# Optimization experiments

Measured on AMD Instinct MI355X. Metric: run time of the kernel, lower is better.

## Reference

```python
import jax, jax.numpy as jnp
import numpy as np

EPS = 1e-5
GROUPS = 32

def group_norm(x, w, b):
    B, C, H, W = x.shape
    g = GROUPS
    xr = x.reshape(B, g, C // g, H * W)
    mean = xr.mean(axis=(2, 3), keepdims=True)
    var = xr.var(axis=(2, 3), keepdims=True)
    h = ((xr - mean) / jnp.sqrt(var + EPS)).reshape(B, C, H, W)
    return h * w[None, :, None, None] + b[None, :, None, None]

def setup_inputs() -> dict:
    key = jax.random.key(0)
    ks = jax.random.split(key, 7)
    B, C, H, W = 8, 256, 64, 64
    d = C // 8  # 32
    x = jax.random.normal(ks[0], (B, C, H, W), dtype=jnp.float32)
    norm_w = 1.0 + 0.1 * jax.random.normal(ks[1], (C,), dtype=jnp.float32)
    norm_b = 0.1 * jax.random.normal(ks[2], (C,), dtype=jnp.float32)
    s = 1.0 / np.sqrt(C)
    Wq = jax.random.normal(ks[3], (d, C), dtype=jnp.float32) * s
    Wk = jax.random.normal(ks[4], (d, C), dtype=jnp.float32) * s
    Wv = jax.random.normal(ks[5], (C, C), dtype=jnp.float32) * s
    Wproj = jax.random.normal(ks[6], (C, C), dtype=jnp.float32) * s
    gamma = jnp.full((1,), 0.5, dtype=jnp.float32)  # torch init is 0; nonzero so attention path contributes
    return {"x": x, "norm_w": norm_w, "norm_b": norm_b, "Wq": Wq, "Wk": Wk,
            "Wv": Wv, "Wproj": Wproj, "gamma": gamma}

def reference(x, norm_w, norm_b, Wq, Wk, Wv, Wproj, gamma):
    B, C, H, W = x.shape
    N = H * W
    h = group_norm(x, norm_w, norm_b)           # (B,C,H,W)
    hf = h.reshape(B, C, N)                      # flatten spatial
    d = Wq.shape[0]
    q = jnp.einsum('dc,bcn->bnd', Wq, hf)        # (B,N,d)
    k = jnp.einsum('dc,bcn->bdn', Wk, hf)        # (B,d,N)
    v = jnp.einsum('oc,bcn->bno', Wv, hf)        # (B,N,C)
    scale = d ** (-0.5)
    attn = jax.nn.softmax(jnp.einsum('bnd,bdm->bnm', q, k) * scale, axis=-1)  # (B,N,N)
    out = jnp.einsum('bnm,bmo->bno', attn, v)    # (B,N,C)
    out = out.transpose(0, 2, 1).reshape(B, C, H, W)
    proj = jnp.einsum('oc,bchw->bohw', Wproj, out)
    return x + gamma[0] * proj
```

## Files before the change

kernel.cpp:

```cpp
#include <hip/hip_runtime.h>
#include <cstdint>


typedef __bf16 bf16x8 __attribute__((ext_vector_type(8)));
typedef float f32x4 __attribute__((ext_vector_type(4)));
typedef float f32x16 __attribute__((ext_vector_type(16)));
typedef unsigned int u32x4 __attribute__((ext_vector_type(4)));
typedef unsigned short u16x4 __attribute__((ext_vector_type(4)));
typedef unsigned short u16x8 __attribute__((ext_vector_type(8)));

#define DEVI __device__ __forceinline__

DEVI unsigned short f2bf(float f) {
    __bf16 h = (__bf16)f;
    return __builtin_bit_cast(unsigned short, h);
}
DEVI float bf2f(unsigned short u) {
    unsigned int x = ((unsigned int)u) << 16;
    return __builtin_bit_cast(float, x);
}

DEVI f32x4 mfma16(bf16x8 a, bf16x8 b, f32x4 c) {
    return __builtin_amdgcn_mfma_f32_16x16x32_bf16(a, b, c, 0, 0, 0);
}
DEVI f32x16 mfma32(bf16x8 a, bf16x8 b, f32x16 c) {
    return __builtin_amdgcn_mfma_f32_32x32x16_bf16(a, b, c, 0, 0, 0);
}

DEVI void glds16(const unsigned short* g, unsigned short* l) {
    const __attribute__((address_space(1))) unsigned int* gp =
        reinterpret_cast<const __attribute__((address_space(1))) unsigned int*>(
            reinterpret_cast<uintptr_t>(g));
    __attribute__((address_space(3))) unsigned int* lp =
        reinterpret_cast<__attribute__((address_space(3))) unsigned int*>(
            reinterpret_cast<uintptr_t>(l));
    __builtin_amdgcn_global_load_lds(gp, lp, 16, 0, 0);
}

DEVI void barrier_raw() {
    asm volatile("" ::: "memory");
    __builtin_amdgcn_s_barrier();
    asm volatile("" ::: "memory");
}
DEVI void wait_vm0() {
    __builtin_amdgcn_s_waitcnt(0x3F70);
}

#define QSCALE 0.2550663133f
#define MFIX   12.0f

__global__ __launch_bounds__(1024) void k_gnorm(
        const float* __restrict__ x, const float* __restrict__ gw,
        const float* __restrict__ gb, unsigned short* __restrict__ ht) {
    int bg = blockIdx.x;
    int b = bg >> 5, g = bg & 31;
    const float* xb = x + ((size_t)(b * 256 + g * 8)) * 4096;
    int t = threadIdx.x;
    int n0 = t * 4;
    f32x4 cv[8];
    #pragma unroll
    for (int c = 0; c < 8; c++) cv[c] = *(const f32x4*)(xb + c * 4096 + n0);
    float s1 = 0.f, s2 = 0.f;
    #pragma unroll
    for (int c = 0; c < 8; c++) {
        #pragma unroll
        for (int j = 0; j < 4; j++) { s1 += cv[c][j]; s2 += cv[c][j] * cv[c][j]; }
    }
    #pragma unroll
    for (int off = 1; off < 64; off <<= 1) {
        s1 += __shfl_xor(s1, off);
        s2 += __shfl_xor(s2, off);
    }
    __shared__ float red[34];
    int wv_ = t >> 6;
    if ((t & 63) == 0) { red[wv_ * 2] = s1; red[wv_ * 2 + 1] = s2; }
    __syncthreads();
    if (t == 0) {
        float a = 0.f, q = 0.f;
        #pragma unroll
        for (int i = 0; i < 16; i++) { a += red[i * 2]; q += red[i * 2 + 1]; }
        float mean = a * (1.f / 32768.f);
        float var = q * (1.f / 32768.f) - mean * mean;
        red[32] = mean; red[33] = rsqrtf(var + 1e-5f);
    }
    __syncthreads();
    float mean = red[32], rstd = red[33];
    float wv8[8], bv8[8];
    #pragma unroll
    for (int c = 0; c < 8; c++) { wv8[c] = gw[g * 8 + c] * rstd; bv8[c] = gb[g * 8 + c] - mean * rstd * gw[g * 8 + c]; }
    #pragma unroll
    for (int j = 0; j < 4; j++) {
        u16x8 pk;
        #pragma unroll
        for (int c = 0; c < 8; c++) pk[c] = f2bf(cv[c][j] * wv8[c] + bv8[c]);
        *(u16x8*)(&ht[((size_t)(b * 4096 + n0 + j)) * 256 + g * 8]) = pk;
    }
}

template <int EPI>
__global__ __launch_bounds__(256) void k_gemm(
        const unsigned short* __restrict__ A, void* __restrict__ outp,
        const float* __restrict__ xres, const float* __restrict__ gamma, int ldout,
        const float* __restrict__ wqf, const float* __restrict__ wkf,
        const float* __restrict__ wvf, void* __restrict__ outp2) {
    __shared__ unsigned short lA[128 * 72];
    __shared__ unsigned short lB[64 * 72];
    int t = threadIdx.x;
    int m0 = blockIdx.x * 128, n0 = blockIdx.y * 64;
    if (EPI == 3) {
        if (blockIdx.y == 0) n0 = 0;
        else n0 = (blockIdx.y - 1) * 64;
    }
    int w = t >> 6, lane = t & 63, l15 = lane & 15, quad = lane >> 4;
    f32x4 z4 = {0.f, 0.f, 0.f, 0.f};
    f32x4 acc[2][4];
    #pragma unroll
    for (int i = 0; i < 2; i++)
        #pragma unroll
        for (int j = 0; j < 4; j++) acc[i][j] = z4;

    auto ldB8 = [&](int row, int gc) -> u16x8 {
        const float* src;
        float sc = 1.f;
        if (EPI == 3) {
            if (blockIdx.y == 0) {
                if (row < 32) { src = wqf + (size_t)row * 256 + gc; sc = QSCALE; }
                else          { src = wkf + (size_t)(row - 32) * 256 + gc; }
            } else {
                src = wvf + (size_t)(n0 + row) * 256 + gc;
            }
        } else {
            src = wvf + (size_t)(n0 + row) * 256 + gc;
        }
        f32x4 a = *(const f32x4*)src;
        f32x4 b2 = *(const f32x4*)(src + 4);
        u16x8 r;
        #pragma unroll
        for (int j = 0; j < 4; j++) { r[j] = f2bf(a[j] * sc); r[4 + j] = f2bf(b2[j] * sc); }
        return r;
    };

    for (int kb = 0; kb < 4; kb++) {
        #pragma unroll
        for (int i = 0; i < 4; i++) {
            int ch = i * 256 + t;
            int row = ch >> 3, col = (ch & 7) * 8;
            u32x4 v = *(const u32x4*)(A + (size_t)(m0 + row) * 256 + kb * 64 + col);
            *(u32x4*)(&lA[row * 72 + col]) = v;
        }
        #pragma unroll
        for (int i = 0; i < 2; i++) {
            int ch = i * 256 + t;
            int row = ch >> 3, col = (ch & 7) * 8;
            u16x8 v = ldB8(row, kb * 64 + col);
            *(u16x8*)(&lB[row * 72 + col]) = v;
        }
        __syncthreads();
        #pragma unroll
        for (int ks = 0; ks < 2; ks++) {
            bf16x8 af[2], bfr[4];
            #pragma unroll
            for (int fr = 0; fr < 2; fr++)
                af[fr] = *(const bf16x8*)(&lA[(w * 32 + fr * 16 + l15) * 72 + ks * 32 + quad * 8]);
            #pragma unroll
            for (int fn = 0; fn < 4; fn++)
                bfr[fn] = *(const bf16x8*)(&lB[(fn * 16 + l15) * 72 + ks * 32 + quad * 8]);
            #pragma unroll
            for (int fr = 0; fr < 2; fr++)
                #pragma unroll
                for (int fn = 0; fn < 4; fn++)
                    acc[fr][fn] = mfma16(af[fr], bfr[fn], acc[fr][fn]);
        }
        __syncthreads();
    }

    bool epi0 = (EPI == 3 && blockIdx.y == 0);
    bool epi1 = (EPI == 3 && blockIdx.y != 0);
    if (epi0) {
        unsigned short* out = (unsigned short*)outp;
        #pragma unroll
        for (int fr = 0; fr < 2; fr++)
            #pragma unroll
            for (int fn = 0; fn < 4; fn++)
                #pragma unroll
                for (int r = 0; r < 4; r++) {
                    int m = m0 + w * 32 + fr * 16 + quad * 4 + r;
                    int n = n0 + fn * 16 + l15;
                    out[(size_t)m * ldout + n] = f2bf(acc[fr][fn][r]);
                }
    } else if (epi1) {
        unsigned short* out = (unsigned short*)outp2;
        int b = m0 >> 12, nb = (m0 & 4095) + w * 32;
        int swq = ((quad & 1) << 1) | (quad >> 1);
        #pragma unroll
        for (int fr = 0; fr < 2; fr++)
            #pragma unroll
            for (int fn = 0; fn < 4; fn++) {
                int o = n0 + fn * 16 + l15;
                int n = nb + fr * 16 + swq * 4;
                u16x4 pk;
                #pragma unroll
                for (int r = 0; r < 4; r++) pk[r] = f2bf(acc[fr][fn][r]);
                *(u16x4*)(&out[(((size_t)(b * 256 + o)) << 12) + n]) = pk;
            }
    } else {
        float* out = (float*)outp;
        float gm = gamma[0];
        int b = m0 >> 12, nb = (m0 & 4095) + w * 32;
        #pragma unroll
        for (int fr = 0; fr < 2; fr++)
            #pragma unroll
            for (int fn = 0; fn < 4; fn++) {
                int o = n0 + fn * 16 + l15;
                int n = nb + fr * 16 + quad * 4;
                size_t base = (((size_t)(b * 256 + o)) << 12) + n;
                f32x4 xv = *(const f32x4*)(xres + base);
                f32x4 ov;
                #pragma unroll
                for (int r = 0; r < 4; r++) ov[r] = xv[r] + gm * acc[fr][fn][r];
                *(f32x4*)(out + base) = ov;
            }
    }
}

__global__ __launch_bounds__(512, 2) void k_flash(
        const unsigned short* __restrict__ QK, const unsigned short* __restrict__ Vt,
        unsigned short* __restrict__ Oa) {
    __shared__ __align__(16) char smem[67584];
    int id = blockIdx.x;
    int b = id & 7;
    int r3 = id >> 3;
    int oh = r3 & 1, qblk = r3 >> 1;
    int t = threadIdx.x, w = t >> 6, ln = t & 63;
    int l31 = ln & 31, h = ln >> 5;
    int qh = w >> 1, kh = w & 1;
    int q0 = qblk * 256 + qh * 64;

    bf16x8 qb0[2], qb1[2];
    #pragma unroll
    for (int qt2 = 0; qt2 < 2; qt2++) {
        const unsigned short* qrow = QK + ((size_t)(b * 4096 + q0 + qt2 * 32 + l31)) * 64;
        qb0[qt2] = *(const bf16x8*)(qrow + h * 8);
        qb1[qt2] = *(const bf16x8*)(qrow + 16 + h * 8);
    }

    int cgK = (ln & 3) ^ ((ln >> 2) & 3) ^ ((ln >> 4) & 3);
    const unsigned short* gK = QK + ((size_t)(b * 4096 + (w & 3) * 16 + (ln >> 2))) * 64 + 32 + cgK * 8;
    int vc8 = (ln & 7) ^ ((ln >> 3) & 7);
    const unsigned short* gV = Vt + (((size_t)(b * 256 + oh * 128 + w * 16 + (ln >> 3))) << 12) + vc8 * 8;

    unsigned short* lK0 = (unsigned short*)smem;
    unsigned short* lV0 = (unsigned short*)(smem + 4096);
    unsigned short* lK1 = (unsigned short*)(smem + 20480);
    unsigned short* lV1 = (unsigned short*)(smem + 24576);
    unsigned short* sK0 = lK0 + (w & 3) * 512;
    unsigned short* sV0 = lV0 + w * 1024;
    unsigned short* sK1 = lK1 + (w & 3) * 512;
    unsigned short* sV1 = lV1 + w * 1024;

    f32x16 z16;
    #pragma unroll
    for (int i = 0; i < 16; i++) z16[i] = 0.f;
    f32x16 minit;
    #pragma unroll
    for (int i = 0; i < 16; i++) minit[i] = -MFIX;
    f32x16 Oacc[2][4];
    #pragma unroll
    for (int qt2 = 0; qt2 < 2; qt2++)
        #pragma unroll
        for (int i = 0; i < 4; i++) Oacc[qt2][i] = z16;
    float lsum[2] = {0.f, 0.f};

    int gl = (l31 & 3) ^ ((l31 >> 2) & 3);
    const unsigned short* kf0p0 = lK0 + (kh * 32 + l31) * 32 + ((0 + h) ^ gl) * 8;
    const unsigned short* kf1p0 = lK0 + (kh * 32 + l31) * 32 + ((2 + h) ^ gl) * 8;
    const unsigned short* kf0p1 = lK1 + (kh * 32 + l31) * 32 + ((0 + h) ^ gl) * 8;
    const unsigned short* kf1p1 = lK1 + (kh * 32 + l31) * 32 + ((2 + h) ^ gl) * 8;
    int slotA = ((kh * 4 + 0 * 2 + h) ^ (ln & 7)) * 8;
    int slotB = ((kh * 4 + 1 * 2 + h) ^ (ln & 7)) * 8;

    auto stage = [&](int kn, unsigned short* sK, unsigned short* sV) {
        if (w < 4) glds16(gK + (size_t)kn * 4096, sK);
        #pragma unroll
        for (int j = 0; j < 2; j++)
            glds16(gV + ((size_t)j * 8 << 12) + kn * 64, sV + j * 512);
    };

    auto compute = [&](const unsigned short* kf0p, const unsigned short* kf1p,
                       const unsigned short* lV) {
        bf16x8 kf0 = *(const bf16x8*)kf0p;
        bf16x8 kf1 = *(const bf16x8*)kf1p;
        bf16x8 pa[2][2];
        #pragma unroll
        for (int qt2 = 0; qt2 < 2; qt2++) {
            f32x16 St = mfma32(kf0, qb0[qt2], minit);
            St = mfma32(kf1, qb1[qt2], St);
            u16x8 p0u, p1u;
            float s = 0.f;
            #pragma unroll
            for (int j = 0; j < 8; j++) {
                float e0 = __builtin_amdgcn_exp2f(St[j]);
                float e1 = __builtin_amdgcn_exp2f(St[8 + j]);
                s += e0 + e1;
                p0u[j] = f2bf(e0);
                p1u[j] = f2bf(e1);
            }
            lsum[qt2] += s;
            pa[qt2][0] = __builtin_bit_cast(bf16x8, p0u);
            pa[qt2][1] = __builtin_bit_cast(bf16x8, p1u);
        }
        __builtin_amdgcn_s_setprio(1);
        #pragma unroll
        for (int nt = 0; nt < 4; nt++) {
            bf16x8 vf = *(const bf16x8*)(lV + (nt * 32 + l31) * 64 + slotA);
            Oacc[0][nt] = mfma32(pa[0][0], vf, Oacc[0][nt]);
            Oacc[1][nt] = mfma32(pa[1][0], vf, Oacc[1][nt]);
        }
        #pragma unroll
        for (int nt = 0; nt < 4; nt++) {
            bf16x8 vf = *(const bf16x8*)(lV + (nt * 32 + l31) * 64 + slotB);
            Oacc[0][nt] = mfma32(pa[0][1], vf, Oacc[0][nt]);
            Oacc[1][nt] = mfma32(pa[1][1], vf, Oacc[1][nt]);
        }
        __builtin_amdgcn_s_setprio(0);
    };

    stage(0, sK0, sV0);
    for (int kt = 0; kt < 64; kt += 2) {
        wait_vm0();
        barrier_raw();
        stage(kt + 1, sK1, sV1);
        compute(kf0p0, kf1p0, lV0);
        wait_vm0();
        barrier_raw();
        if (kt + 2 < 64) stage(kt + 2, sK0, sV0);
        compute(kf0p1, kf1p1, lV1);
    }
    #pragma unroll
    for (int qt2 = 0; qt2 < 2; qt2++) lsum[qt2] += __shfl_xor(lsum[qt2], 32);
    __syncthreads();

    float* sf = (float*)smem;
    int lbase = (kh ? 16384 : 16640) + qh * 64 + l31;
    sf[lbase] = lsum[0];
    sf[lbase + 32] = lsum[1];
    if (kh == 1) {
        #pragma unroll
        for (int qt2 = 0; qt2 < 2; qt2++)
            #pragma unroll
            for (int nt = 0; nt < 4; nt++)
                #pragma unroll
                for (int rg = 0; rg < 2; rg++) {
                    u16x8 pk;
                    #pragma unroll
                    for (int j = 0; j < 8; j++) pk[j] = f2bf(Oacc[qt2][nt][rg * 8 + j]);
                    *(u16x8*)(smem + qh * 16384 + qt2 * 8192 + nt * 2048 + rg * 1024 + ln * 16) = pk;
                }
    }
    __syncthreads();
    if (kh == 0) {
        #pragma unroll
        for (int qt2 = 0; qt2 < 2; qt2++) {
            float rl[16];
            #pragma unroll
            for (int r = 0; r < 16; r++) {
                int row = (r & 3) + 8 * (r >> 2) + 4 * h;
                float l = sf[16384 + qh * 64 + qt2 * 32 + row] +
                          sf[16640 + qh * 64 + qt2 * 32 + row];
                rl[r] = 1.f / l;
            }
            size_t rb = (size_t)(b * 4096 + qblk * 256 + qh * 64 + qt2 * 32);
            #pragma unroll
            for (int nt = 0; nt < 4; nt++)
                #pragma unroll
                for (int rg = 0; rg < 2; rg++) {
                    u16x8 pk = *(const u16x8*)(smem + qh * 16384 + qt2 * 8192 + nt * 2048 + rg * 1024 + ln * 16);
                    #pragma unroll
                    for (int j = 0; j < 8; j++) {
                        int r = rg * 8 + j;
                        float val = (Oacc[qt2][nt][r] + bf2f(pk[j])) * rl[r];
                        int row = (r & 3) + 8 * (r >> 2) + 4 * h;
                        Oa[(rb + row) * 256 + oh * 128 + nt * 32 + l31] = f2bf(val);
                    }
                }
        }
    }
}

extern "C" void kernel_launch(void* const* d_in, const int* in_sizes, int n_in,
                              void* d_out, int out_size, void* d_ws, size_t ws_size,
                              hipStream_t stream) {
    const float* x  = (const float*)d_in[0];
    const float* nw = (const float*)d_in[1];
    const float* nb = (const float*)d_in[2];
    const float* wq = (const float*)d_in[3];
    const float* wk = (const float*)d_in[4];
    const float* wv = (const float*)d_in[5];
    const float* wp = (const float*)d_in[6];
    const float* gm = (const float*)d_in[7];

    char* p = (char*)d_ws;
    unsigned short* ht  = (unsigned short*)p; p += (size_t)32768 * 256 * 2;
    unsigned short* qk  = (unsigned short*)p; p += (size_t)32768 * 64 * 2;
    unsigned short* vt  = (unsigned short*)p; p += (size_t)8 * 256 * 4096 * 2;
    unsigned short* oa  = (unsigned short*)p; p += (size_t)32768 * 256 * 2;

    k_gnorm<<<dim3(256), dim3(1024), 0, stream>>>(x, nw, nb, ht);
    k_gemm<3><<<dim3(256, 5), dim3(256), 0, stream>>>(ht, (void*)qk, nullptr, nullptr, 64, wq, wk, wv, (void*)vt);
    k_flash<<<dim3(256), dim3(512), 0, stream>>>(qk, vt, oa);
    k_gemm<2><<<dim3(256, 4), dim3(256), 0, stream>>>(oa, d_out, x, gm, 0, nullptr, nullptr, wp, nullptr);
}
```

Baseline: 223.5 us.

## Triple-buffer K/V LDS staging with partial vmcnt waits in attention loop

Replaces the double-buffered K/V staging in the attention main loop with three LDS buffers. Each step prefetches two tiles ahead and waits only for the oldest tile's loads, using vmcnt thresholds of 3 or 2 depending on whether the wave also loads K. The aim is to hide more global-load latency behind the MFMA and softmax work. In exchange it uses more LDS, which may lower occupancy, and it needs a tail step for the last tile.

```diff
diff --git a/kernel.cpp b/kernel.cpp
--- a/kernel.cpp
+++ b/kernel.cpp
@@ -42,9 +42,9 @@
     __builtin_amdgcn_s_barrier();
     asm volatile("" ::: "memory");
 }
-DEVI void wait_vm0() {
-    __builtin_amdgcn_s_waitcnt(0x3F70);
-}
+DEVI void wait_vm0() { __builtin_amdgcn_s_waitcnt(0x3F70); }
+DEVI void wait_vm2() { __builtin_amdgcn_s_waitcnt(0x3F72); }
+DEVI void wait_vm3() { __builtin_amdgcn_s_waitcnt(0x3F73); }
 
 #define QSCALE 0.2550663133f
 #define MFIX   12.0f
@@ -249,14 +249,18 @@
     int vc8 = (ln & 7) ^ ((ln >> 3) & 7);
     const unsigned short* gV = Vt + (((size_t)(b * 256 + oh * 128 + w * 16 + (ln >> 3))) << 12) + vc8 * 8;
 
-    unsigned short* lK0 = (unsigned short*)smem;
-    unsigned short* lV0 = (unsigned short*)(smem + 4096);
-    unsigned short* lK1 = (unsigned short*)(smem + 20480);
-    unsigned short* lV1 = (unsigned short*)(smem + 24576);
-    unsigned short* sK0 = lK0 + (w & 3) * 512;
-    unsigned short* sV0 = lV0 + w * 1024;
-    unsigned short* sK1 = lK1 + (w & 3) * 512;
-    unsigned short* sV1 = lV1 + w * 1024;
+    unsigned short* const Kb0 = (unsigned short*)smem;
+    unsigned short* const Kb1 = (unsigned short*)(smem + 4096);
+    unsigned short* const Kb2 = (unsigned short*)(smem + 8192);
+    unsigned short* const Vb0 = (unsigned short*)(smem + 12288);
+    unsigned short* const Vb1 = (unsigned short*)(smem + 28672);
+    unsigned short* const Vb2 = (unsigned short*)(smem + 45056);
+    unsigned short* const sK0 = Kb0 + (w & 3) * 512;
+    unsigned short* const sK1 = Kb1 + (w & 3) * 512;
+    unsigned short* const sK2 = Kb2 + (w & 3) * 512;
+    unsigned short* const sV0 = Vb0 + w * 1024;
+    unsigned short* const sV1 = Vb1 + w * 1024;
+    unsigned short* const sV2 = Vb2 + w * 1024;
 
     f32x16 z16;
     #pragma unroll
@@ -272,10 +276,14 @@
     float lsum[2] = {0.f, 0.f};
 
     int gl = (l31 & 3) ^ ((l31 >> 2) & 3);
-    const unsigned short* kf0p0 = lK0 + (kh * 32 + l31) * 32 + ((0 + h) ^ gl) * 8;
-    const unsigned short* kf1p0 = lK0 + (kh * 32 + l31) * 32 + ((2 + h) ^ gl) * 8;
-    const unsigned short* kf0p1 = lK1 + (kh * 32 + l31) * 32 + ((0 + h) ^ gl) * 8;
-    const unsigned short* kf1p1 = lK1 + (kh * 32 + l31) * 32 + ((2 + h) ^ gl) * 8;
+    const int koff0 = (kh * 32 + l31) * 32 + ((0 + h) ^ gl) * 8;
+    const int koff1 = (kh * 32 + l31) * 32 + ((2 + h) ^ gl) * 8;
+    const unsigned short* const kp0_0 = Kb0 + koff0;
+    const unsigned short* const kp1_0 = Kb0 + koff1;
+    const unsigned short* const kp0_1 = Kb1 + koff0;
+    const unsigned short* const kp1_1 = Kb1 + koff1;
+    const unsigned short* const kp0_2 = Kb2 + koff0;
+    const unsigned short* const kp1_2 = Kb2 + koff1;
     int slotA = ((kh * 4 + 0 * 2 + h) ^ (ln & 7)) * 8;
     int slotB = ((kh * 4 + 1 * 2 + h) ^ (ln & 7)) * 8;
 
@@ -284,6 +292,9 @@
         #pragma unroll
         for (int j = 0; j < 2; j++)
             glds16(gV + ((size_t)j * 8 << 12) + kn * 64, sV + j * 512);
+    };
+    auto waitL = [&]() {
+        if (w < 4) wait_vm3(); else wait_vm2();
     };
 
     auto compute = [&](const unsigned short* kf0p, const unsigned short* kf1p,
@@ -326,16 +337,22 @@
     };
 
     stage(0, sK0, sV0);
-    for (int kt = 0; kt < 64; kt += 2) {
-        wait_vm0();
-        barrier_raw();
-        stage(kt + 1, sK1, sV1);
-        compute(kf0p0, kf1p0, lV0);
-        wait_vm0();
-        barrier_raw();
-        if (kt + 2 < 64) stage(kt + 2, sK0, sV0);
-        compute(kf0p1, kf1p1, lV1);
-    }
+    stage(1, sK1, sV1);
+
+    for (int kt = 0; kt < 63; kt += 3) {
+        waitL(); barrier_raw();
+        stage(kt + 2, sK2, sV2);
+        compute(kp0_0, kp1_0, Vb0);
+        waitL(); barrier_raw();
+        stage(kt + 3, sK0, sV0);
+        compute(kp0_1, kp1_1, Vb1);
+        waitL(); barrier_raw();
+        if (kt + 4 < 64) stage(kt + 4, sK1, sV1);
+        compute(kp0_2, kp1_2, Vb2);
+    }
+    wait_vm0(); barrier_raw();
+    compute(kp0_0, kp1_0, Vb0);
+
     #pragma unroll
     for (int qt2 = 0; qt2 < 2; qt2++) lsum[qt2] += __shfl_xor(lsum[qt2], 32);
     __syncthreads();
```

New measurement: 286.4 us. +28.1%, slower.
